# Kernel tuning notes

Measured on AMD Instinct MI355X. Metric: run time of the kernel, lower is better.

Reference implementation:

```python
import jax, jax.numpy as jnp
import numpy as np

B, S, OUT = 128, 3000, 84
CODE_SEQ = 30
LAT = 1024
C, D = 128, 16
CB = C * D  # 2048
IN = CODE_SEQ * OUT  # 2520


def setup_inputs() -> dict:
    key = jax.random.key(0)
    ks = jax.random.split(key, 16)
    def w(k, shape):
        fan_in = shape[0]
        return (jax.random.normal(k, shape, dtype=jnp.float32) / np.sqrt(fan_in)).astype(jnp.float32)
    return {
        "y": jax.random.normal(ks[0], (B, S, OUT), dtype=jnp.float32),
        "emb": jax.random.uniform(ks[1], (C, D), minval=-1.0 / C, maxval=1.0 / C, dtype=jnp.float32),
        "eW1": w(ks[2], (IN, LAT)), "eb1": jnp.zeros((LAT,), jnp.float32),
        "eW2": w(ks[3], (LAT, LAT)), "eb2": jnp.zeros((LAT,), jnp.float32),
        "eW3": w(ks[4], (LAT, CB)), "eb3": jnp.zeros((CB,), jnp.float32),
        "dW1": w(ks[5], (CB, LAT)), "db1": jnp.zeros((LAT,), jnp.float32),
        "dW2": w(ks[6], (LAT, LAT)), "db2": jnp.zeros((LAT,), jnp.float32),
        "dW3": w(ks[7], (LAT, IN)), "db3": jnp.zeros((IN,), jnp.float32),
    }


def _mlp(z, W1, b1, W2, b2, W3, b3):
    # LinearEncoder in eval mode (dropout = identity): Linear->ELU->Linear->ELU->Linear
    z = jax.nn.elu(z @ W1 + b1)
    z = jax.nn.elu(z @ W2 + b2)
    return z @ W3 + b3


def reference(y, emb, eW1, eb1, eW2, eb2, eW3, eb3, dW1, db1, dW2, db2, dW3, db3):
    batch, seq_len = y.shape[0], y.shape[1]
    # seq_len % code_seq == 0 -> padding branch is a no-op
    y2 = y.reshape(batch, -1, IN)                 # (B, n_m, 2520)
    n_m = y2.shape[1]
    ze = _mlp(y2, eW1, eb1, eW2, eb2, eW3, eb3)   # (B, n_m, 2048)
    zef = ze.reshape(batch, n_m, -1, D)           # (B, n_m, G=128, 16)
    # squared L2 distance to each of C codes, without materializing (B,n_m,G,C,D)
    dist = (
        jnp.sum(zef ** 2, -1, keepdims=True)
        - 2.0 * jnp.einsum("bngd,cd->bngc", zef, emb)
        + jnp.sum(emb ** 2, -1)
    )                                             # (B, n_m, G, C)
    nn_idx = jnp.argmin(dist, -1)                 # (B, n_m, G)
    zq = emb[nn_idx].reshape(batch, n_m, -1)      # (B, n_m, 2048)
    dec_in = ze + jax.lax.stop_gradient(zq - ze)  # straight-through
    out = _mlp(dec_in, dW1, db1, dW2, db2, dW3, db3)
    out = out.reshape(batch, -1, OUT)[:, :seq_len, :]
    return (out, ze, zq)
```

## Files before the change

kernel.cpp:

```cpp
#include <hip/hip_runtime.h>
#include <hip/hip_bf16.h>
#include <cstdint>
#include <cstddef>

typedef __bf16 bf16_t;
typedef bf16_t bf16x8 __attribute__((ext_vector_type(8)));
typedef float  f32x4  __attribute__((ext_vector_type(4)));

__device__ __forceinline__ void gl_lds16(const void* g, void* l) {
  __builtin_amdgcn_global_load_lds(
      (const __attribute__((address_space(1))) void*)g,
      (__attribute__((address_space(3))) void*)l, 16, 0, 0);
}

#define BAR()  __builtin_amdgcn_s_barrier()
#define LGK0() asm volatile("s_waitcnt lgkmcnt(0)" ::: "memory")

__global__ __launch_bounds__(256) void transpose_w(
    const float* __restrict__ W, bf16_t* __restrict__ Wt,
    int K, int N, int Kpad, int Npad)
{
  __shared__ float tile[32][33];
  const int tx = threadIdx.x, ty = threadIdx.y;
  const int k0 = blockIdx.x * 32, n0 = blockIdx.y * 32;
#pragma unroll
  for (int i = 0; i < 4; ++i) {
    int k = k0 + ty + i * 8, n = n0 + tx;
    tile[ty + i * 8][tx] = (k < K && n < N) ? W[(size_t)k * N + n] : 0.f;
  }
  __syncthreads();
#pragma unroll
  for (int i = 0; i < 4; ++i) {
    int n = n0 + ty + i * 8, k = k0 + tx;
    if (n < Npad && k < Kpad)
      Wt[(size_t)n * Kpad + k] = (bf16_t)tile[tx][ty + i * 8];
  }
}

__global__ __launch_bounds__(256) void pack_x0(
    const float* __restrict__ y, bf16_t* __restrict__ X0)
{
  const int idx = blockIdx.x * 256 + threadIdx.x;
  const int r = idx / 320, c = (idx % 320) * 8;
  bf16x8 v;
  if (c < 2520) {
    const float4 f0 = *(const float4*)(y + (size_t)r * 2520 + c);
    const float4 f1 = *(const float4*)(y + (size_t)r * 2520 + c + 4);
    v[0] = (bf16_t)f0.x; v[1] = (bf16_t)f0.y; v[2] = (bf16_t)f0.z; v[3] = (bf16_t)f0.w;
    v[4] = (bf16_t)f1.x; v[5] = (bf16_t)f1.y; v[6] = (bf16_t)f1.z; v[7] = (bf16_t)f1.w;
  } else {
#pragma unroll
    for (int j = 0; j < 8; ++j) v[j] = (bf16_t)0.f;
  }
  *(bf16x8*)(X0 + (size_t)r * 2560 + c) = v;
}

__device__ __forceinline__ bf16x8 ldsfrag(const bf16_t* half_, int r, int kc, int kg) {
  int lin = (r << 7) + (kc << 6) + (kg << 4);
  lin ^= ((lin >> 9) & 1) << 5;
  return *(const bf16x8*)((const char*)half_ + lin);
}

template<int ELU>
__global__ __launch_bounds__(512, 2) void gemm256(
    const bf16_t* __restrict__ A, const bf16_t* __restrict__ Bt,
    const float* __restrict__ bias,
    bf16_t* __restrict__ Cb, float* __restrict__ Cf,
    int M, int N, int K, int Nlog)
{
  __shared__ __align__(16) bf16_t lds[65536];

  const int t  = threadIdx.x;
  const int w  = t >> 6, l = t & 63;
  const int fr = l & 15, kg = l >> 4;
  const int wm = (w >> 2) * 128, wn = (w & 3) * 64;
  const int bro = (wn & 64);

  const int gx = gridDim.x;
  const int nwg = gx * (int)gridDim.y;
  int lin = blockIdx.y * gx + blockIdx.x;
  int q8 = nwg >> 3, r8 = nwg & 7, xcd = lin & 7, idx = lin >> 3;
  int swz = (xcd < r8 ? xcd * (q8 + 1) : r8 * (q8 + 1) + (xcd - r8) * q8) + idx;
  const int tn = (swz % gx) * 256;
  const int tm = (swz / gx) * 256;

  const int srow = w * 8 + (l >> 3);
  const int sce  = ((l & 7) * 8) ^ (((l >> 5) & 1) << 4);
  const int sdst = w * 512 + l * 8;

  const int NT = K >> 6;

  f32x4 acc[8][4];
#pragma unroll
  for (int i = 0; i < 8; ++i)
#pragma unroll
    for (int j = 0; j < 4; ++j) acc[i][j] = (f32x4){0.f, 0.f, 0.f, 0.f};

  auto stage = [&](const bf16_t* gbase, bf16_t* lhalf) {
    gl_lds16(gbase + (size_t)srow * K + sce,        lhalf + sdst);
    gl_lds16(gbase + (size_t)(srow + 64) * K + sce, lhalf + 4096 + sdst);
  };

  stage(A  + (size_t)tm * K,          lds);
  stage(A  + (size_t)(tm + 128) * K,  lds + 8192);
  stage(Bt + (size_t)tn * K,          lds + 16384);
  stage(Bt + (size_t)(tn + 128) * K,  lds + 16384 + 8192);
  asm volatile("s_waitcnt vmcnt(0)" ::: "memory");
  BAR();

  for (int kt = 0; kt < NT; ++kt) {
    const int s = kt & 1;
    const bf16_t* aH = lds + s * 32768 + (wm >> 7) * 8192;
    const bf16_t* bH = lds + s * 32768 + 16384 + (wn >> 7) * 8192;
    bf16_t* aNx = lds + (s ^ 1) * 32768;
    bf16_t* bNx = aNx + 16384;
    const bool pf = (kt + 1 < NT);
    const size_t kn = (size_t)(kt + 1) << 6;

    bf16x8 af[4][2], bf_[2][2];

#pragma unroll
    for (int mi = 0; mi < 4; ++mi)
#pragma unroll
      for (int kc = 0; kc < 2; ++kc)
        af[mi][kc] = ldsfrag(aH, mi * 16 + fr, kc, kg);
#pragma unroll
    for (int nj = 0; nj < 2; ++nj)
#pragma unroll
      for (int kc = 0; kc < 2; ++kc)
        bf_[nj][kc] = ldsfrag(bH, bro + nj * 16 + fr, kc, kg);
    if (pf) {
      stage(A + (size_t)tm * K + kn,         aNx);
      stage(A + (size_t)(tm + 128) * K + kn, aNx + 8192);
    }
    BAR(); LGK0();
    __builtin_amdgcn_s_setprio(1);
#pragma unroll
    for (int mi = 0; mi < 4; ++mi)
#pragma unroll
      for (int nj = 0; nj < 2; ++nj)
#pragma unroll
        for (int kc = 0; kc < 2; ++kc)
          acc[mi][nj] = __builtin_amdgcn_mfma_f32_16x16x32_bf16(af[mi][kc], bf_[nj][kc], acc[mi][nj], 0, 0, 0);
    __builtin_amdgcn_s_setprio(0);
    BAR();

#pragma unroll
    for (int nj = 0; nj < 2; ++nj)
#pragma unroll
      for (int kc = 0; kc < 2; ++kc)
        bf_[nj][kc] = ldsfrag(bH, bro + (nj + 2) * 16 + fr, kc, kg);
    if (pf) {
      stage(Bt + (size_t)tn * K + kn,         bNx);
      stage(Bt + (size_t)(tn + 128) * K + kn, bNx + 8192);
    }
    BAR(); LGK0();
    __builtin_amdgcn_s_setprio(1);
#pragma unroll
    for (int mi = 0; mi < 4; ++mi)
#pragma unroll
      for (int nj = 0; nj < 2; ++nj)
#pragma unroll
        for (int kc = 0; kc < 2; ++kc)
          acc[mi][nj + 2] = __builtin_amdgcn_mfma_f32_16x16x32_bf16(af[mi][kc], bf_[nj][kc], acc[mi][nj + 2], 0, 0, 0);
    __builtin_amdgcn_s_setprio(0);
    BAR();

#pragma unroll
    for (int mi = 0; mi < 4; ++mi)
#pragma unroll
      for (int kc = 0; kc < 2; ++kc)
        af[mi][kc] = ldsfrag(aH, (mi + 4) * 16 + fr, kc, kg);
    BAR(); LGK0();
    __builtin_amdgcn_s_setprio(1);
#pragma unroll
    for (int mi = 0; mi < 4; ++mi)
#pragma unroll
      for (int nj = 0; nj < 2; ++nj)
#pragma unroll
        for (int kc = 0; kc < 2; ++kc)
          acc[mi + 4][nj + 2] = __builtin_amdgcn_mfma_f32_16x16x32_bf16(af[mi][kc], bf_[nj][kc], acc[mi + 4][nj + 2], 0, 0, 0);
    __builtin_amdgcn_s_setprio(0);
    BAR();

#pragma unroll
    for (int nj = 0; nj < 2; ++nj)
#pragma unroll
      for (int kc = 0; kc < 2; ++kc)
        bf_[nj][kc] = ldsfrag(bH, bro + nj * 16 + fr, kc, kg);
    BAR(); LGK0();
    __builtin_amdgcn_s_setprio(1);
#pragma unroll
    for (int mi = 0; mi < 4; ++mi)
#pragma unroll
      for (int nj = 0; nj < 2; ++nj)
#pragma unroll
        for (int kc = 0; kc < 2; ++kc)
          acc[mi + 4][nj] = __builtin_amdgcn_mfma_f32_16x16x32_bf16(af[mi][kc], bf_[nj][kc], acc[mi + 4][nj], 0, 0, 0);
    __builtin_amdgcn_s_setprio(0);
    if (pf) asm volatile("s_waitcnt vmcnt(0)" ::: "memory");
    BAR();
  }

#pragma unroll
  for (int mi = 0; mi < 8; ++mi) {
    const int row0 = tm + wm + mi * 16 + kg * 4;
#pragma unroll
    for (int nj = 0; nj < 4; ++nj) {
      const int col = tn + wn + nj * 16 + fr;
      const float bv = (col < Nlog) ? bias[col] : 0.f;
#pragma unroll
      for (int r = 0; r < 4; ++r) {
        float v = acc[mi][nj][r] + bv;
        if (ELU) v = (v > 0.f) ? v : expm1f(v);
        const int row = row0 + r;
        if (Cb) Cb[(size_t)row * N + col] = (bf16_t)v;
        if (Cf && col < Nlog) Cf[(size_t)row * Nlog + col] = v;
      }
    }
  }
}

__global__ __launch_bounds__(256) void vq_kernel(
    const float* __restrict__ ze, const float* __restrict__ emb,
    float* __restrict__ zq, bf16_t* __restrict__ zqb)
{
  __shared__ float se[2048];
  __shared__ float sh[128];
  const int t = threadIdx.x;
  for (int i = t; i < 2048; i += 256) se[i] = emb[i];
  __syncthreads();
  if (t < 128) {
    float s = 0.f;
#pragma unroll
    for (int j = 0; j < 16; ++j) { float v = se[t * 16 + j]; s += v * v; }
    sh[t] = 0.5f * s;
  }
  __syncthreads();

  const size_t g0 = (size_t)blockIdx.x * 1024 + t;
  float z[4][16];
#pragma unroll
  for (int q = 0; q < 4; ++q) {
    const float4* p = (const float4*)(ze + (g0 + q * 256) * 16);
#pragma unroll
    for (int v = 0; v < 4; ++v) {
      float4 f = p[v];
      z[q][v * 4 + 0] = f.x; z[q][v * 4 + 1] = f.y;
      z[q][v * 4 + 2] = f.z; z[q][v * 4 + 3] = f.w;
    }
  }

  int   best[4] = {0, 0, 0, 0};
  float bd[4]   = {1e30f, 1e30f, 1e30f, 1e30f};
  for (int c = 0; c < 128; ++c) {
    float e[16];
    const float4* ep = (const float4*)(se + c * 16);
#pragma unroll
    for (int v = 0; v < 4; ++v) {
      float4 f = ep[v];
      e[v * 4 + 0] = f.x; e[v * 4 + 1] = f.y; e[v * 4 + 2] = f.z; e[v * 4 + 3] = f.w;
    }
    const float h = sh[c];
#pragma unroll
    for (int q = 0; q < 4; ++q) {
      float d = h;
#pragma unroll
      for (int j = 0; j < 16; ++j) d = fmaf(-z[q][j], e[j], d);
      if (d < bd[q]) { bd[q] = d; best[q] = c; }
    }
  }

#pragma unroll
  for (int q = 0; q < 4; ++q) {
    const float* e = se + best[q] * 16;
    float4* o = (float4*)(zq + (g0 + q * 256) * 16);
#pragma unroll
    for (int v = 0; v < 4; ++v) o[v] = ((const float4*)e)[v];
    bf16x8 b0, b1;
#pragma unroll
    for (int j = 0; j < 8; ++j) { b0[j] = (bf16_t)e[j]; b1[j] = (bf16_t)e[j + 8]; }
    *(bf16x8*)(zqb + (g0 + q * 256) * 16)     = b0;
    *(bf16x8*)(zqb + (g0 + q * 256) * 16 + 8) = b1;
  }
}

extern "C" void kernel_launch(void* const* d_in, const int* in_sizes, int n_in,
                              void* d_out, int out_size, void* d_ws, size_t ws_size,
                              hipStream_t stream)
{
  const float* y   = (const float*)d_in[0];
  const float* emb = (const float*)d_in[1];
  const float* eW1 = (const float*)d_in[2];
  const float* eb1 = (const float*)d_in[3];
  const float* eW2 = (const float*)d_in[4];
  const float* eb2 = (const float*)d_in[5];
  const float* eW3 = (const float*)d_in[6];
  const float* eb3 = (const float*)d_in[7];
  const float* dW1 = (const float*)d_in[8];
  const float* db1 = (const float*)d_in[9];
  const float* dW2 = (const float*)d_in[10];
  const float* db2 = (const float*)d_in[11];
  const float* dW3 = (const float*)d_in[12];
  const float* db3 = (const float*)d_in[13];

  float* out = (float*)d_out;
  float* ze  = out + 32256000;
  float* zq  = ze + 26214400;

  uint8_t* ws = (uint8_t*)d_ws;
  size_t off = 0;
  auto alloc = [&](size_t bytes) -> void* {
    void* p = ws + off; off += (bytes + 255) & ~(size_t)255; return p;
  };
  bf16_t* X0  = (bf16_t*)alloc(12800ULL * 2560 * 2);
  bf16_t* W1t = (bf16_t*)alloc(1024ULL * 2560 * 2);
  bf16_t* W2t = (bf16_t*)alloc(1024ULL * 1024 * 2);
  bf16_t* W3t = (bf16_t*)alloc(2048ULL * 1024 * 2);
  bf16_t* V1t = (bf16_t*)alloc(1024ULL * 2048 * 2);
  bf16_t* V2t = (bf16_t*)alloc(1024ULL * 1024 * 2);
  bf16_t* V3t = (bf16_t*)alloc(2560ULL * 1024 * 2);
  bf16_t* H1  = (bf16_t*)alloc(12800ULL * 1024 * 2);
  bf16_t* H2  = (bf16_t*)alloc(12800ULL * 1024 * 2);
  bf16_t* ZQb = (bf16_t*)alloc(12800ULL * 2048 * 2);

  const dim3 tb(32, 8);
  transpose_w<<<dim3(80, 32), tb, 0, stream>>>(eW1, W1t, 2520, 1024, 2560, 1024);
  transpose_w<<<dim3(32, 32), tb, 0, stream>>>(eW2, W2t, 1024, 1024, 1024, 1024);
  transpose_w<<<dim3(32, 64), tb, 0, stream>>>(eW3, W3t, 1024, 2048, 1024, 2048);
  transpose_w<<<dim3(64, 32), tb, 0, stream>>>(dW1, V1t, 2048, 1024, 2048, 1024);
  transpose_w<<<dim3(32, 32), tb, 0, stream>>>(dW2, V2t, 1024, 1024, 1024, 1024);
  transpose_w<<<dim3(32, 80), tb, 0, stream>>>(dW3, V3t, 1024, 2520, 1024, 2560);

  pack_x0<<<16000, 256, 0, stream>>>(y, X0);

  gemm256<1><<<dim3(4, 50), 512, 0, stream>>>(X0, W1t, eb1, H1, nullptr, 12800, 1024, 2560, 1024);
  gemm256<1><<<dim3(4, 50), 512, 0, stream>>>(H1, W2t, eb2, H2, nullptr, 12800, 1024, 1024, 1024);
  gemm256<0><<<dim3(8, 50), 512, 0, stream>>>(H2, W3t, eb3, nullptr, ze, 12800, 2048, 1024, 2048);
  vq_kernel<<<1600, 256, 0, stream>>>(ze, emb, zq, ZQb);
  gemm256<1><<<dim3(4, 50), 512, 0, stream>>>(ZQb, V1t, db1, H1, nullptr, 12800, 1024, 2048, 1024);
  gemm256<1><<<dim3(4, 50), 512, 0, stream>>>(H1, V2t, db2, H2, nullptr, 12800, 1024, 1024, 1024);
  gemm256<0><<<dim3(10, 50), 512, 0, stream>>>(H2, V3t, db3, nullptr, out, 12800, 2560, 1024, 2520);
}
```

Measured before the change: 674.2 us.

## Fuse prep launches, spread GEMM prefetch across phases, use MFMA for VQ search

Merges the six weight transposes and the input pack into one prep kernel, removing six launches. In the GEMM main loop, the four next-tile stage calls are spread across the four MFMA phases with finer vmcnt waits, so global loads overlap more compute. The VQ nearest-code search now runs on bf16 MFMA instead of scalar fp32 FMAs, with a wave-shuffle argmin. That computes distances in bf16 and can flip argmin choices on near-ties compared with the fp32 reference.

```diff
diff --git a/kernel.cpp b/kernel.cpp
--- a/kernel.cpp
+++ b/kernel.cpp
@@ -16,13 +16,13 @@
 #define BAR()  __builtin_amdgcn_s_barrier()
 #define LGK0() asm volatile("s_waitcnt lgkmcnt(0)" ::: "memory")
 
-__global__ __launch_bounds__(256) void transpose_w(
+__device__ __forceinline__ void transpose_tile(
     const float* __restrict__ W, bf16_t* __restrict__ Wt,
-    int K, int N, int Kpad, int Npad)
+    int K, int N, int Kpad, int Npad, int bx, int by, int t)
 {
   __shared__ float tile[32][33];
-  const int tx = threadIdx.x, ty = threadIdx.y;
-  const int k0 = blockIdx.x * 32, n0 = blockIdx.y * 32;
+  const int tx = t & 31, ty = t >> 5;
+  const int k0 = bx * 32, n0 = by * 32;
 #pragma unroll
   for (int i = 0; i < 4; ++i) {
     int k = k0 + ty + i * 8, n = n0 + tx;
@@ -37,22 +37,45 @@
   }
 }
 
-__global__ __launch_bounds__(256) void pack_x0(
-    const float* __restrict__ y, bf16_t* __restrict__ X0)
-{
-  const int idx = blockIdx.x * 256 + threadIdx.x;
-  const int r = idx / 320, c = (idx % 320) * 8;
-  bf16x8 v;
-  if (c < 2520) {
-    const float4 f0 = *(const float4*)(y + (size_t)r * 2520 + c);
-    const float4 f1 = *(const float4*)(y + (size_t)r * 2520 + c + 4);
-    v[0] = (bf16_t)f0.x; v[1] = (bf16_t)f0.y; v[2] = (bf16_t)f0.z; v[3] = (bf16_t)f0.w;
-    v[4] = (bf16_t)f1.x; v[5] = (bf16_t)f1.y; v[6] = (bf16_t)f1.z; v[7] = (bf16_t)f1.w;
-  } else {
-#pragma unroll
-    for (int j = 0; j < 8; ++j) v[j] = (bf16_t)0.f;
-  }
-  *(bf16x8*)(X0 + (size_t)r * 2560 + c) = v;
+__global__ __launch_bounds__(256) void prep_kernel(
+    const float* __restrict__ y, bf16_t* __restrict__ X0,
+    const float* __restrict__ eW1, bf16_t* __restrict__ W1t,
+    const float* __restrict__ eW2, bf16_t* __restrict__ W2t,
+    const float* __restrict__ eW3, bf16_t* __restrict__ W3t,
+    const float* __restrict__ dW1, bf16_t* __restrict__ V1t,
+    const float* __restrict__ dW2, bf16_t* __restrict__ V2t,
+    const float* __restrict__ dW3, bf16_t* __restrict__ V3t)
+{
+  const int b = blockIdx.x;
+  const int t = threadIdx.x;
+  if (b < 16000) {
+    const int idx = b * 256 + t;
+    const int r = idx / 320, c = (idx % 320) * 8;
+    bf16x8 v;
+    if (c < 2520) {
+      const float4 f0 = *(const float4*)(y + (size_t)r * 2520 + c);
+      const float4 f1 = *(const float4*)(y + (size_t)r * 2520 + c + 4);
+      v[0] = (bf16_t)f0.x; v[1] = (bf16_t)f0.y; v[2] = (bf16_t)f0.z; v[3] = (bf16_t)f0.w;
+      v[4] = (bf16_t)f1.x; v[5] = (bf16_t)f1.y; v[6] = (bf16_t)f1.z; v[7] = (bf16_t)f1.w;
+    } else {
+#pragma unroll
+      for (int j = 0; j < 8; ++j) v[j] = (bf16_t)0.f;
+    }
+    *(bf16x8*)(X0 + (size_t)r * 2560 + c) = v;
+    return;
+  }
+  int lb = b - 16000;
+  if (lb < 2560)      { transpose_tile(eW1, W1t, 2520, 1024, 2560, 1024, lb % 80, lb / 80, t); return; }
+  lb -= 2560;
+  if (lb < 1024)      { transpose_tile(eW2, W2t, 1024, 1024, 1024, 1024, lb % 32, lb / 32, t); return; }
+  lb -= 1024;
+  if (lb < 2048)      { transpose_tile(eW3, W3t, 1024, 2048, 1024, 2048, lb % 32, lb / 32, t); return; }
+  lb -= 2048;
+  if (lb < 2048)      { transpose_tile(dW1, V1t, 2048, 1024, 2048, 1024, lb % 64, lb / 64, t); return; }
+  lb -= 2048;
+  if (lb < 1024)      { transpose_tile(dW2, V2t, 1024, 1024, 1024, 1024, lb % 32, lb / 32, t); return; }
+  lb -= 1024;
+  transpose_tile(dW3, V3t, 1024, 2520, 1024, 2560, lb % 32, lb / 32, t);
 }
 
 __device__ __forceinline__ bf16x8 ldsfrag(const bf16_t* half_, int r, int kc, int kg) {
@@ -124,15 +147,14 @@
 #pragma unroll
       for (int kc = 0; kc < 2; ++kc)
         af[mi][kc] = ldsfrag(aH, mi * 16 + fr, kc, kg);
+    asm volatile("s_waitcnt vmcnt(0)" ::: "memory");
+    BAR();
 #pragma unroll
     for (int nj = 0; nj < 2; ++nj)
 #pragma unroll
       for (int kc = 0; kc < 2; ++kc)
         bf_[nj][kc] = ldsfrag(bH, bro + nj * 16 + fr, kc, kg);
-    if (pf) {
-      stage(A + (size_t)tm * K + kn,         aNx);
-      stage(A + (size_t)(tm + 128) * K + kn, aNx + 8192);
-    }
+    if (pf) stage(A + (size_t)tm * K + kn, aNx);
     BAR(); LGK0();
     __builtin_amdgcn_s_setprio(1);
 #pragma unroll
@@ -150,10 +172,7 @@
 #pragma unroll
       for (int kc = 0; kc < 2; ++kc)
         bf_[nj][kc] = ldsfrag(bH, bro + (nj + 2) * 16 + fr, kc, kg);
-    if (pf) {
-      stage(Bt + (size_t)tn * K + kn,         bNx);
-      stage(Bt + (size_t)(tn + 128) * K + kn, bNx + 8192);
-    }
+    if (pf) stage(A + (size_t)(tm + 128) * K + kn, aNx + 8192);
     BAR(); LGK0();
     __builtin_amdgcn_s_setprio(1);
 #pragma unroll
@@ -171,6 +190,7 @@
 #pragma unroll
       for (int kc = 0; kc < 2; ++kc)
         af[mi][kc] = ldsfrag(aH, (mi + 4) * 16 + fr, kc, kg);
+    if (pf) stage(Bt + (size_t)tn * K + kn, bNx);
     BAR(); LGK0();
     __builtin_amdgcn_s_setprio(1);
 #pragma unroll
@@ -188,6 +208,8 @@
 #pragma unroll
       for (int kc = 0; kc < 2; ++kc)
         bf_[nj][kc] = ldsfrag(bH, bro + nj * 16 + fr, kc, kg);
+    if (pf) stage(Bt + (size_t)(tn + 128) * K + kn, bNx + 8192);
+    asm volatile("s_waitcnt vmcnt(4)" ::: "memory");
     BAR(); LGK0();
     __builtin_amdgcn_s_setprio(1);
 #pragma unroll
@@ -198,7 +220,6 @@
         for (int kc = 0; kc < 2; ++kc)
           acc[mi + 4][nj] = __builtin_amdgcn_mfma_f32_16x16x32_bf16(af[mi][kc], bf_[nj][kc], acc[mi + 4][nj], 0, 0, 0);
     __builtin_amdgcn_s_setprio(0);
-    if (pf) asm volatile("s_waitcnt vmcnt(0)" ::: "memory");
     BAR();
   }
 
@@ -221,67 +242,96 @@
   }
 }
 
-__global__ __launch_bounds__(256) void vq_kernel(
+__global__ __launch_bounds__(256) void vq_mfma(
     const float* __restrict__ ze, const float* __restrict__ emb,
     float* __restrict__ zq, bf16_t* __restrict__ zqb)
 {
-  __shared__ float se[2048];
-  __shared__ float sh[128];
+  __shared__ float  se[2048];
+  __shared__ bf16_t seb[2048];
   const int t = threadIdx.x;
-  for (int i = t; i < 2048; i += 256) se[i] = emb[i];
+  for (int i = t; i < 2048; i += 256) { float v = emb[i]; se[i] = v; seb[i] = (bf16_t)v; }
   __syncthreads();
-  if (t < 128) {
+
+  const int l = t & 63, w = t >> 6;
+  const int col = l & 15;
+  const int ks8 = (l >> 4) * 8;
+  const bool kact = (ks8 < 16);
+
+  bf16x8 bfrag[8];
+  float  hv[8];
+#pragma unroll
+  for (int cb = 0; cb < 8; ++cb) {
     float s = 0.f;
-#pragma unroll
-    for (int j = 0; j < 16; ++j) { float v = se[t * 16 + j]; s += v * v; }
-    sh[t] = 0.5f * s;
-  }
-  __syncthreads();
-
-  const size_t g0 = (size_t)blockIdx.x * 1024 + t;
-  float z[4][16];
-#pragma unroll
-  for (int q = 0; q < 4; ++q) {
-    const float4* p = (const float4*)(ze + (g0 + q * 256) * 16);
-#pragma unroll
-    for (int v = 0; v < 4; ++v) {
-      float4 f = p[v];
-      z[q][v * 4 + 0] = f.x; z[q][v * 4 + 1] = f.y;
-      z[q][v * 4 + 2] = f.z; z[q][v * 4 + 3] = f.w;
-    }
-  }
-
-  int   best[4] = {0, 0, 0, 0};
-  float bd[4]   = {1e30f, 1e30f, 1e30f, 1e30f};
-  for (int c = 0; c < 128; ++c) {
-    float e[16];
-    const float4* ep = (const float4*)(se + c * 16);
-#pragma unroll
-    for (int v = 0; v < 4; ++v) {
-      float4 f = ep[v];
-      e[v * 4 + 0] = f.x; e[v * 4 + 1] = f.y; e[v * 4 + 2] = f.z; e[v * 4 + 3] = f.w;
-    }
-    const float h = sh[c];
-#pragma unroll
-    for (int q = 0; q < 4; ++q) {
-      float d = h;
-#pragma unroll
-      for (int j = 0; j < 16; ++j) d = fmaf(-z[q][j], e[j], d);
-      if (d < bd[q]) { bd[q] = d; best[q] = c; }
-    }
-  }
-
-#pragma unroll
-  for (int q = 0; q < 4; ++q) {
-    const float* e = se + best[q] * 16;
-    float4* o = (float4*)(zq + (g0 + q * 256) * 16);
-#pragma unroll
-    for (int v = 0; v < 4; ++v) o[v] = ((const float4*)e)[v];
-    bf16x8 b0, b1;
-#pragma unroll
-    for (int j = 0; j < 8; ++j) { b0[j] = (bf16_t)e[j]; b1[j] = (bf16_t)e[j + 8]; }
-    *(bf16x8*)(zqb + (g0 + q * 256) * 16)     = b0;
-    *(bf16x8*)(zqb + (g0 + q * 256) * 16 + 8) = b1;
+    bf16x8 bf;
+#pragma unroll
+    for (int j = 0; j < 8; ++j) bf[j] = (bf16_t)0.f;
+    if (kact) {
+      const float* ep = se + (cb * 16 + col) * 16 + ks8;
+      float4 e0 = *(const float4*)ep;
+      float4 e1 = *(const float4*)(ep + 4);
+      bf[0] = (bf16_t)e0.x; bf[1] = (bf16_t)e0.y; bf[2] = (bf16_t)e0.z; bf[3] = (bf16_t)e0.w;
+      bf[4] = (bf16_t)e1.x; bf[5] = (bf16_t)e1.y; bf[6] = (bf16_t)e1.z; bf[7] = (bf16_t)e1.w;
+      s = e0.x*e0.x + e0.y*e0.y + e0.z*e0.z + e0.w*e0.w
+        + e1.x*e1.x + e1.y*e1.y + e1.z*e1.z + e1.w*e1.w;
+    }
+    s += __shfl_xor(s, 16);
+    s += __shfl_xor(s, 32);
+    bfrag[cb] = bf;
+    hv[cb] = 0.5f * s;
+  }
+
+  const int base_tile = blockIdx.x * 64 + w * 16;
+  for (int it = 0; it < 16; ++it) {
+    const int tile = base_tile + it;
+    const int row = tile >> 3, g0 = (tile & 7) * 16;
+
+    bf16x8 afrag;
+#pragma unroll
+    for (int j = 0; j < 8; ++j) afrag[j] = (bf16_t)0.f;
+    if (kact) {
+      const float* ap = ze + (size_t)row * 2048 + (g0 + col) * 16 + ks8;
+      float4 a0 = *(const float4*)ap;
+      float4 a1 = *(const float4*)(ap + 4);
+      afrag[0] = (bf16_t)(-a0.x); afrag[1] = (bf16_t)(-a0.y);
+      afrag[2] = (bf16_t)(-a0.z); afrag[3] = (bf16_t)(-a0.w);
+      afrag[4] = (bf16_t)(-a1.x); afrag[5] = (bf16_t)(-a1.y);
+      afrag[6] = (bf16_t)(-a1.z); afrag[7] = (bf16_t)(-a1.w);
+    }
+
+    f32x4 dd[8];
+#pragma unroll
+    for (int cb = 0; cb < 8; ++cb) {
+      f32x4 c = (f32x4){hv[cb], hv[cb], hv[cb], hv[cb]};
+      dd[cb] = __builtin_amdgcn_mfma_f32_16x16x32_bf16(afrag, bfrag[cb], c, 0, 0, 0);
+    }
+
+#pragma unroll
+    for (int r = 0; r < 4; ++r) {
+      float bd = dd[0][r]; int bi = col;
+#pragma unroll
+      for (int cb = 1; cb < 8; ++cb) {
+        float v = dd[cb][r];
+        int   ci = cb * 16 + col;
+        if (v < bd) { bd = v; bi = ci; }
+      }
+#pragma unroll
+      for (int m = 1; m < 16; m <<= 1) {
+        float od = __shfl_xor(bd, m);
+        int   oi = __shfl_xor(bi, m);
+        if (od < bd || (od == bd && oi < bi)) { bd = od; bi = oi; }
+      }
+      if (col == r) {
+        const int tok = (l >> 4) * 4 + r;
+        const size_t go = ((size_t)row * 128 + g0 + tok) * 16;
+        const float*  e  = se  + bi * 16;
+        const bf16_t* eb = seb + bi * 16;
+#pragma unroll
+        for (int v = 0; v < 4; ++v)
+          *(float4*)(zq + go + v * 4) = ((const float4*)e)[v];
+        *(bf16x8*)(zqb + go)     = ((const bf16x8*)eb)[0];
+        *(bf16x8*)(zqb + go + 8) = ((const bf16x8*)eb)[1];
+      }
+    }
   }
 }
 
@@ -324,20 +374,13 @@
   bf16_t* H2  = (bf16_t*)alloc(12800ULL * 1024 * 2);
   bf16_t* ZQb = (bf16_t*)alloc(12800ULL * 2048 * 2);
 
-  const dim3 tb(32, 8);
-  transpose_w<<<dim3(80, 32), tb, 0, stream>>>(eW1, W1t, 2520, 1024, 2560, 1024);
-  transpose_w<<<dim3(32, 32), tb, 0, stream>>>(eW2, W2t, 1024, 1024, 1024, 1024);
-  transpose_w<<<dim3(32, 64), tb, 0, stream>>>(eW3, W3t, 1024, 2048, 1024, 2048);
-  transpose_w<<<dim3(64, 32), tb, 0, stream>>>(dW1, V1t, 2048, 1024, 2048, 1024);
-  transpose_w<<<dim3(32, 32), tb, 0, stream>>>(dW2, V2t, 1024, 1024, 1024, 1024);
-  transpose_w<<<dim3(32, 80), tb, 0, stream>>>(dW3, V3t, 1024, 2520, 1024, 2560);
-
-  pack_x0<<<16000, 256, 0, stream>>>(y, X0);
+  prep_kernel<<<27264, 256, 0, stream>>>(y, X0, eW1, W1t, eW2, W2t, eW3, W3t,
+                                         dW1, V1t, dW2, V2t, dW3, V3t);
 
   gemm256<1><<<dim3(4, 50), 512, 0, stream>>>(X0, W1t, eb1, H1, nullptr, 12800, 1024, 2560, 1024);
   gemm256<1><<<dim3(4, 50), 512, 0, stream>>>(H1, W2t, eb2, H2, nullptr, 12800, 1024, 1024, 1024);
   gemm256<0><<<dim3(8, 50), 512, 0, stream>>>(H2, W3t, eb3, nullptr, ze, 12800, 2048, 1024, 2048);
-  vq_kernel<<<1600, 256, 0, stream>>>(ze, emb, zq, ZQb);
+  vq_mfma<<<1600, 256, 0, stream>>>(ze, emb, zq, ZQb);
   gemm256<1><<<dim3(4, 50), 512, 0, stream>>>(ZQb, V1t, db1, H1, nullptr, 12800, 1024, 2048, 1024);
   gemm256<1><<<dim3(4, 50), 512, 0, stream>>>(H1, V2t, db2, H2, nullptr, 12800, 1024, 1024, 1024);
   gemm256<0><<<dim3(10, 50), 512, 0, stream>>>(H2, V3t, db3, nullptr, out, 12800, 2560, 1024, 2520);
```

After: 679.6 us. Within noise of the previous version (+0.8%).
